# Performance work log

Hardware: AMD Instinct MI355X
Metric: run time of the kernel (lower is better)

Reference implementation:

```python
import jax, jax.numpy as jnp
import numpy as np

EPS = 1e-12

def t5_layer_norm(x, w):
    # T5-style RMS norm: no mean subtraction, no bias
    var = jnp.mean(x * x, axis=-1, keepdims=True)
    return x * jax.lax.rsqrt(var + EPS) * w

def gether(h, a2, t2):
    # a2: [B,S,1,1] (row similarity), t2: [B,1,S,1] (col similarity)
    h_y = h * t2
    h_left  = jnp.pad(h_y, ((0,0),(0,0),(1,0),(0,0)))[:, :, :-1, :]
    h_right = jnp.pad(h_y, ((0,0),(0,0),(0,1),(0,0)))[:, :, 1:, :]
    h_x = h * a2
    h_up   = jnp.pad(h_x, ((0,0),(1,0),(0,0),(0,0)))[:, :-1, :, :]
    h_down = jnp.pad(h_x, ((0,0),(0,1),(0,0),(0,0)))[:, 1:, :, :]
    return h + h_left + h_right + h_up + h_down

def syntax_gether(h, dep_weights):
    h_dep = h * dep_weights            # [B,S,S,D]
    h_in = jnp.sum(h_dep, axis=2)      # [B,S,D]
    h_out = jnp.sum(h_dep, axis=1)     # [B,S,D]
    return h_in[:, :, None, :] + h_out[:, None, :, :]

def feature_fusion(sem, syn, gate_w, gate_b):
    combined = jnp.concatenate([sem, syn], axis=-1)
    gate = jax.nn.sigmoid(combined @ gate_w + gate_b)
    return gate * sem + (1.0 - gate) * syn

def setup_inputs() -> dict:
    key = jax.random.key(0)
    ks = jax.random.split(key, 16)
    B, S, D_in, D_out = 4, 96, 768, 256
    N_DEP, D_DEP = 44, 6
    inp = {
        "table": jax.random.normal(ks[0], (B, S, S, D_in), dtype=jnp.float32),
        "a_simi": jax.random.uniform(ks[1], (B, S), dtype=jnp.float32),
        "t_simi": jax.random.uniform(ks[2], (B, S), dtype=jnp.float32),
        "dep_matrix": jax.random.randint(ks[3], (B, S, S), 0, 2).astype(jnp.float32),
        "dep_types": jax.random.randint(ks[4], (B, S, S), 0, N_DEP).astype(jnp.int32),
        # parameters (torch Linear weights stored transposed: [in, out])
        "dense1_w": jax.random.normal(ks[5], (D_in, D_in), dtype=jnp.float32) * 0.02,
        "dense1_b": jnp.zeros((D_in,), dtype=jnp.float32),
        "dense2_w": jax.random.normal(ks[6], (D_in, D_out), dtype=jnp.float32) * 0.02,
        "dense2_b": jnp.zeros((D_out,), dtype=jnp.float32),
        "dep_emb": jax.random.normal(ks[7], (N_DEP, D_DEP), dtype=jnp.float32) * 0.02,
        "dep_att_w": jax.random.normal(ks[8], (D_DEP, 1), dtype=jnp.float32) * 0.02,
        "dep_att_b": jnp.zeros((1,), dtype=jnp.float32),
        "gate_w": jax.random.normal(ks[9], (2 * D_in, D_in), dtype=jnp.float32) * 0.02,
        "gate_b": jnp.zeros((D_in,), dtype=jnp.float32),
        "norm1_w": jnp.ones((D_in,), dtype=jnp.float32),
        "norm2_w": jnp.ones((D_out,), dtype=jnp.float32),
    }
    return inp

def reference(table, a_simi, t_simi, dep_matrix, dep_types,
              dense1_w, dense1_b, dense2_w, dense2_b,
              dep_emb, dep_att_w, dep_att_b, gate_w, gate_b,
              norm1_w, norm2_w):
    a2 = a_simi[:, :, None, None]   # [B,S,1,1]
    t2 = t_simi[:, None, :, None]   # [B,1,S,1]
    dep_embeds = dep_emb[dep_types]                       # [B,S,S,6]
    dep_weights = jax.nn.sigmoid(dep_embeds @ dep_att_w + dep_att_b)
    dep_weights = dep_weights * dep_matrix[..., None]     # [B,S,S,1]

    h0 = table
    h1_sem = gether(h0, a2, t2)
    h1_syn = syntax_gether(h0, dep_weights)
    h1 = feature_fusion(h1_sem, h1_syn, gate_w, gate_b)
    h1 = jax.nn.relu(t5_layer_norm((h1 + h0) @ dense1_w + dense1_b, norm1_w))

    h2_sem = gether(h1, a2, t2)
    h2_syn = syntax_gether(h1, dep_weights)
    h2 = feature_fusion(h2_sem, h2_syn, gate_w, gate_b)
    h2 = jax.nn.relu(t5_layer_norm((h2 + h1) @ dense2_w + dense2_b, norm2_w))
    return h2
```

## Files before the change

kernel.cpp:

```cpp
#include <hip/hip_runtime.h>
#include <cstdint>
#include <cstddef>

#define SDIM 96
#define BDIM 4
#define NROWS (BDIM * SDIM * SDIM)
#define BSROWS (BDIM * SDIM)
#define DIN 768
#define DOUT 256

typedef short s16x8 __attribute__((ext_vector_type(8)));
typedef float f32x4 __attribute__((ext_vector_type(4)));
typedef unsigned short ushort_t;
typedef unsigned int uint_t;

__device__ __forceinline__ float sigmoid_f(float x) { return 1.0f / (1.0f + expf(-x)); }

__device__ __forceinline__ ushort_t f2bf(float x) {
    uint_t u = __float_as_uint(x);
    u = u + 0x7fffu + ((u >> 16) & 1u);
    return (ushort_t)(u >> 16);
}
__device__ __forceinline__ float bf2f(ushort_t h) {
    return __uint_as_float(((uint_t)h) << 16);
}

__device__ __forceinline__ void split_store(float x, ushort_t* __restrict__ ph,
                                            ushort_t* __restrict__ pl) {
    ushort_t h = f2bf(x);
    *ph = h;
    *pl = f2bf(x - bf2f(h));
}

__device__ __forceinline__ void load_lds16(const void* g, void* l) {
    __builtin_amdgcn_global_load_lds((const __attribute__((address_space(1))) uint_t*)g,
                                     (__attribute__((address_space(3))) uint_t*)l, 16, 0, 0);
}

__global__ __launch_bounds__(256) void depw_k(const int* __restrict__ types,
                                              const float* __restrict__ dmat,
                                              const float* __restrict__ emb,
                                              const float* __restrict__ aw,
                                              const float* __restrict__ ab,
                                              float* __restrict__ Wd) {
    int idx = blockIdx.x * 256 + threadIdx.x;
    if (idx >= NROWS) return;
    int t = types[idx];
    float s = ab[0];
#pragma unroll
    for (int k = 0; k < 6; ++k) s = fmaf(emb[t * 6 + k], aw[k], s);
    Wd[idx] = dmat[idx] * sigmoid_f(s);
}

__global__ __launch_bounds__(256) void splitT_k(const float* __restrict__ W,
                                                ushort_t* __restrict__ TH,
                                                ushort_t* __restrict__ TL, int K, int N) {
    int k = blockIdx.x * 256 + threadIdx.x;
    int n = blockIdx.y;
    if (k >= K) return;
    float x = W[(size_t)k * N + n];
    split_store(x, &TH[(size_t)n * K + k], &TL[(size_t)n * K + k]);
}

__global__ __launch_bounds__(256) void rowsum_k(const float* __restrict__ h,
                                                const float* __restrict__ W,
                                                float* __restrict__ hinF,
                                                ushort_t* __restrict__ hinH,
                                                ushort_t* __restrict__ hinL) {
    int d = blockIdx.x * 256 + threadIdx.x;
    int bi = blockIdx.y;
    const float* hp = h + (size_t)bi * SDIM * DIN + d;
    const float* wp = W + bi * SDIM;
    float acc = 0.f;
#pragma unroll 8
    for (int j = 0; j < SDIM; ++j) acc = fmaf(wp[j], hp[(size_t)j * DIN], acc);
    size_t o = (size_t)bi * DIN + d;
    hinF[o] = acc;
    split_store(acc, &hinH[o], &hinL[o]);
}

__global__ __launch_bounds__(256) void colsum_k(const float* __restrict__ h,
                                                const float* __restrict__ W,
                                                float* __restrict__ houtF,
                                                ushort_t* __restrict__ houtH,
                                                ushort_t* __restrict__ houtL) {
    int d = blockIdx.x * 256 + threadIdx.x;
    int bj = blockIdx.y;
    int b = bj / SDIM;
    int j = bj - b * SDIM;
    const float* hp = h + ((size_t)(b * SDIM) * SDIM + j) * DIN + d;
    const float* wp = W + (size_t)(b * SDIM) * SDIM + j;
    float acc = 0.f;
#pragma unroll 8
    for (int i = 0; i < SDIM; ++i)
        acc = fmaf(wp[(size_t)i * SDIM], hp[(size_t)i * SDIM * DIN], acc);
    size_t o = (size_t)bj * DIN + d;
    houtF[o] = acc;
    split_store(acc, &houtH[o], &houtL[o]);
}

__global__ __launch_bounds__(256) void sem_k(const float* __restrict__ h,
                                             const float* __restrict__ a_simi,
                                             const float* __restrict__ t_simi,
                                             ushort_t* __restrict__ semH,
                                             ushort_t* __restrict__ semL) {
    int idx = blockIdx.x * 256 + threadIdx.x;
    int d4 = idx % 192;
    int m = idx / 192;
    int j = m % SDIM;
    int r = m / SDIM;
    int i = r % SDIM;
    int b = r / SDIM;
    const float4* h4 = (const float4*)h;
    float4 acc = h4[(size_t)m * 192 + d4];
    if (j > 0) {
        float t = t_simi[b * SDIM + j - 1];
        float4 v = h4[(size_t)(m - 1) * 192 + d4];
        acc.x = fmaf(t, v.x, acc.x); acc.y = fmaf(t, v.y, acc.y);
        acc.z = fmaf(t, v.z, acc.z); acc.w = fmaf(t, v.w, acc.w);
    }
    if (j < SDIM - 1) {
        float t = t_simi[b * SDIM + j + 1];
        float4 v = h4[(size_t)(m + 1) * 192 + d4];
        acc.x = fmaf(t, v.x, acc.x); acc.y = fmaf(t, v.y, acc.y);
        acc.z = fmaf(t, v.z, acc.z); acc.w = fmaf(t, v.w, acc.w);
    }
    if (i > 0) {
        float a = a_simi[b * SDIM + i - 1];
        float4 v = h4[(size_t)(m - SDIM) * 192 + d4];
        acc.x = fmaf(a, v.x, acc.x); acc.y = fmaf(a, v.y, acc.y);
        acc.z = fmaf(a, v.z, acc.z); acc.w = fmaf(a, v.w, acc.w);
    }
    if (i < SDIM - 1) {
        float a = a_simi[b * SDIM + i + 1];
        float4 v = h4[(size_t)(m + SDIM) * 192 + d4];
        acc.x = fmaf(a, v.x, acc.x); acc.y = fmaf(a, v.y, acc.y);
        acc.z = fmaf(a, v.z, acc.z); acc.w = fmaf(a, v.w, acc.w);
    }
    size_t o = (size_t)m * DIN + d4 * 4;
    ushort_t hh[4], ll[4];
    float vv[4] = {acc.x, acc.y, acc.z, acc.w};
#pragma unroll
    for (int e = 0; e < 4; ++e) {
        hh[e] = f2bf(vv[e]);
        ll[e] = f2bf(vv[e] - bf2f(hh[e]));
    }
    *(ushort4*)&semH[o] = make_ushort4(hh[0], hh[1], hh[2], hh[3]);
    *(ushort4*)&semL[o] = make_ushort4(ll[0], ll[1], ll[2], ll[3]);
}

template <int EPI>
__global__ __launch_bounds__(256) void gemm_mfma(
    const ushort_t* __restrict__ AH, const ushort_t* __restrict__ AL,
    const ushort_t* __restrict__ BH, const ushort_t* __restrict__ BL,
    int M, int N, int K, int nbx,
    float* __restrict__ C, const float* __restrict__ bias,
    ushort_t* __restrict__ XH, ushort_t* __restrict__ XL,
    const float* __restrict__ Pin, const float* __restrict__ Pout,
    const float* __restrict__ hin, const float* __restrict__ hout,
    const float* __restrict__ hprev) {
    __shared__ __align__(16) ushort_t Ash[2][4096];
    __shared__ __align__(16) ushort_t Asl[2][4096];
    __shared__ __align__(16) ushort_t Bsh[2][4096];
    __shared__ __align__(16) ushort_t Bsl[2][4096];

    const int nwg = gridDim.x;
    const int orig = blockIdx.x;
    const int qq = nwg >> 3, rr = nwg & 7;
    const int xcd = orig & 7, sidx = orig >> 3;
    const int swz = (xcd < rr ? xcd * (qq + 1) : rr * (qq + 1) + (xcd - rr) * qq) + sidx;
    const int bx = swz % nbx;
    const int by = swz / nbx;
    const int bm = by * 128, bn = bx * 128;

    const int tid = threadIdx.x;
    const int wave = tid >> 6, lane = tid & 63;
    const int lq = lane & 15;
    const int lg = lane >> 4;
    const int wm = wave >> 1, wn = wave & 1;

    f32x4 acc[4][4];
#pragma unroll
    for (int a = 0; a < 4; ++a)
#pragma unroll
        for (int b = 0; b < 4; ++b) acc[a][b] = (f32x4){0.f, 0.f, 0.f, 0.f};

    const int nt = K >> 5;

#define STAGE(buf, k0)                                                              \
    {                                                                               \
        _Pragma("unroll") for (int cc = 0; cc < 2; ++cc) {                          \
            const int c = wave + cc * 4;                                            \
            const int row = c * 16 + lq;                                            \
            const size_t ga = (size_t)(bm + row) * K + (k0) + lg * 8;               \
            const size_t gb = (size_t)(bn + row) * K + (k0) + lg * 8;               \
            load_lds16(AH + ga, &Ash[buf][c * 512]);                                \
            load_lds16(AL + ga, &Asl[buf][c * 512]);                                \
            load_lds16(BH + gb, &Bsh[buf][c * 512]);                                \
            load_lds16(BL + gb, &Bsl[buf][c * 512]);                                \
        }                                                                           \
    }

    STAGE(0, 0);
    __syncthreads();

    int cur = 0;
    for (int t = 0; t < nt; ++t) {
        if (t + 1 < nt) STAGE(cur ^ 1, (t + 1) * 32);

        s16x8 ah[4], al[4], bh[4], bl[4];
#pragma unroll
        for (int f = 0; f < 4; ++f) {
            const int cA = (wm * 4 + f) * 512 + lane * 8;
            const int cB = (wn * 4 + f) * 512 + lane * 8;
            ah[f] = *(const s16x8*)&Ash[cur][cA];
            al[f] = *(const s16x8*)&Asl[cur][cA];
            bh[f] = *(const s16x8*)&Bsh[cur][cB];
            bl[f] = *(const s16x8*)&Bsl[cur][cB];
        }
        __builtin_amdgcn_s_setprio(1);
#pragma unroll
        for (int mf = 0; mf < 4; ++mf)
#pragma unroll
            for (int nf = 0; nf < 4; ++nf) {
                acc[mf][nf] = __builtin_amdgcn_mfma_f32_16x16x32_bf16(ah[mf], bh[nf], acc[mf][nf], 0, 0, 0);
                acc[mf][nf] = __builtin_amdgcn_mfma_f32_16x16x32_bf16(ah[mf], bl[nf], acc[mf][nf], 0, 0, 0);
                acc[mf][nf] = __builtin_amdgcn_mfma_f32_16x16x32_bf16(al[mf], bh[nf], acc[mf][nf], 0, 0, 0);
            }
        __builtin_amdgcn_s_setprio(0);
        __syncthreads();
        cur ^= 1;
    }
#undef STAGE

#pragma unroll
    for (int mf = 0; mf < 4; ++mf) {
#pragma unroll
        for (int jj = 0; jj < 4; ++jj) {
            const int gr = bm + wm * 64 + mf * 16 + lg * 4 + jj;
            int ri = 0, rj = 0;
            if (EPI == 1) {
                const int b_ = gr / 9216;
                const int rem = gr - b_ * 9216;
                const int i_ = rem / 96;
                const int j_ = rem - i_ * 96;
                ri = (b_ * 96 + i_) * 768;
                rj = (b_ * 96 + j_) * 768;
            }
#pragma unroll
            for (int nf = 0; nf < 4; ++nf) {
                const int gc = bn + wn * 64 + nf * 16 + lq;
                float v = acc[mf][nf][jj];
                if (EPI == 0) {
                    if (bias != nullptr) v += bias[gc];
                    C[(size_t)gr * N + gc] = v;
                } else {
                    const float gte = sigmoid_f(v + Pin[ri + gc] + Pout[rj + gc]);
                    const float syn = hin[ri + gc] + hout[rj + gc];
                    const size_t o = (size_t)gr * 768 + gc;
                    const float sem = bf2f(AH[o]) + bf2f(AL[o]);
                    const float x = fmaf(gte, sem - syn, syn) + hprev[o];
                    split_store(x, &XH[o], &XL[o]);
                }
            }
        }
    }
}

template <int D>
__global__ __launch_bounds__(256) void norm_relu_k(const float* __restrict__ Y,
                                                   const float* __restrict__ w,
                                                   float* __restrict__ out) {
    constexpr int E = D / 256;
    int row = blockIdx.x;
    int tid = threadIdx.x;
    float v[E];
    float ss = 0.f;
#pragma unroll
    for (int e = 0; e < E; ++e) {
        v[e] = Y[(size_t)row * D + e * 256 + tid];
        ss = fmaf(v[e], v[e], ss);
    }
#pragma unroll
    for (int off = 32; off >= 1; off >>= 1) ss += __shfl_down(ss, off);
    __shared__ float red[4];
    int lane = tid & 63;
    int wid = tid >> 6;
    if (lane == 0) red[wid] = ss;
    __syncthreads();
    float tot = red[0] + red[1] + red[2] + red[3];
    float scale = rsqrtf(tot / (float)D + 1e-12f);
#pragma unroll
    for (int e = 0; e < E; ++e) {
        float o = v[e] * scale * w[e * 256 + tid];
        out[(size_t)row * D + e * 256 + tid] = fmaxf(o, 0.f);
    }
}

extern "C" void kernel_launch(void* const* d_in, const int* in_sizes, int n_in,
                              void* d_out, int out_size, void* d_ws, size_t ws_size,
                              hipStream_t stream) {
    (void)in_sizes; (void)n_in; (void)out_size; (void)ws_size;
    const float* table = (const float*)d_in[0];
    const float* a_simi = (const float*)d_in[1];
    const float* t_simi = (const float*)d_in[2];
    const float* dep_matrix = (const float*)d_in[3];
    const int* dep_types = (const int*)d_in[4];
    const float* d1w = (const float*)d_in[5];
    const float* d1b = (const float*)d_in[6];
    const float* d2w = (const float*)d_in[7];
    const float* d2b = (const float*)d_in[8];
    const float* dep_emb = (const float*)d_in[9];
    const float* att_w = (const float*)d_in[10];
    const float* att_b = (const float*)d_in[11];
    const float* gate_w = (const float*)d_in[12];
    const float* gate_b = (const float*)d_in[13];
    const float* nw1 = (const float*)d_in[14];
    const float* nw2 = (const float*)d_in[15];
    float* out = (float*)d_out;

    char* ws = (char*)d_ws;
    size_t off = 0;
    float* Wd = (float*)(ws + off); off += 147456;
    float* hinF = (float*)(ws + off); off += 1179648;
    float* houtF = (float*)(ws + off); off += 1179648;
    float* Pin = (float*)(ws + off); off += 1179648;
    float* Pout = (float*)(ws + off); off += 1179648;
    ushort_t* hinH = (ushort_t*)(ws + off); off += 589824;
    ushort_t* hinL = (ushort_t*)(ws + off); off += 589824;
    ushort_t* houtH = (ushort_t*)(ws + off); off += 589824;
    ushort_t* houtL = (ushort_t*)(ws + off); off += 589824;
    ushort_t* GtopTH = (ushort_t*)(ws + off); off += 1179648;
    ushort_t* GtopTL = (ushort_t*)(ws + off); off += 1179648;
    ushort_t* GbotTH = (ushort_t*)(ws + off); off += 1179648;
    ushort_t* GbotTL = (ushort_t*)(ws + off); off += 1179648;
    ushort_t* D1TH = (ushort_t*)(ws + off); off += 1179648;
    ushort_t* D1TL = (ushort_t*)(ws + off); off += 1179648;
    ushort_t* D2TH = (ushort_t*)(ws + off); off += 393216;
    ushort_t* D2TL = (ushort_t*)(ws + off); off += 393216;
    char* P1 = ws + off; off += 113246208;
    char* P2 = ws + off; off += 113246208;
    char* P3 = ws + off; off += 113246208;

    const size_t HALF = 56623104;
    ushort_t* S1H = (ushort_t*)P1;            ushort_t* S1L = (ushort_t*)(P1 + HALF);
    ushort_t* X1H = (ushort_t*)P2;            ushort_t* X1L = (ushort_t*)(P2 + HALF);
    float* Y1 = (float*)P1;
    float* h1 = (float*)P3;
    ushort_t* S2H = (ushort_t*)P2;            ushort_t* S2L = (ushort_t*)(P2 + HALF);
    ushort_t* X2H = (ushort_t*)P1;            ushort_t* X2L = (ushort_t*)(P1 + HALF);
    float* Y2 = (float*)P3;

    const dim3 blk(256);
    const dim3 gSplit768(3, 768);
    const dim3 gSplit256(3, 256);
    const dim3 gRS(DIN / 256, BSROWS);
    const int gSem = (NROWS * (DIN / 4)) / 256;
    const int gBig = (NROWS / 128) * (DIN / 128);
    const int gD2g = (NROWS / 128) * (DOUT / 128);
    const int gP = (BSROWS / 128) * (DIN / 128);

    depw_k<<<NROWS / 256, blk, 0, stream>>>(dep_types, dep_matrix, dep_emb, att_w, att_b, Wd);
    splitT_k<<<gSplit768, blk, 0, stream>>>(gate_w, GtopTH, GtopTL, DIN, DIN);
    splitT_k<<<gSplit768, blk, 0, stream>>>(gate_w + (size_t)DIN * DIN, GbotTH, GbotTL, DIN, DIN);
    splitT_k<<<gSplit768, blk, 0, stream>>>(d1w, D1TH, D1TL, DIN, DIN);
    splitT_k<<<gSplit256, blk, 0, stream>>>(d2w, D2TH, D2TL, DIN, DOUT);

    rowsum_k<<<gRS, blk, 0, stream>>>(table, Wd, hinF, hinH, hinL);
    colsum_k<<<gRS, blk, 0, stream>>>(table, Wd, houtF, houtH, houtL);
    sem_k<<<gSem, blk, 0, stream>>>(table, a_simi, t_simi, S1H, S1L);
    gemm_mfma<0><<<gP, blk, 0, stream>>>(hinH, hinL, GbotTH, GbotTL, BSROWS, DIN, DIN, DIN / 128,
                                         Pin, gate_b, nullptr, nullptr, nullptr, nullptr, nullptr, nullptr, nullptr);
    gemm_mfma<0><<<gP, blk, 0, stream>>>(houtH, houtL, GbotTH, GbotTL, BSROWS, DIN, DIN, DIN / 128,
                                         Pout, nullptr, nullptr, nullptr, nullptr, nullptr, nullptr, nullptr, nullptr);
    gemm_mfma<1><<<gBig, blk, 0, stream>>>(S1H, S1L, GtopTH, GtopTL, NROWS, DIN, DIN, DIN / 128,
                                           nullptr, nullptr, X1H, X1L, Pin, Pout, hinF, houtF, table);
    gemm_mfma<0><<<gBig, blk, 0, stream>>>(X1H, X1L, D1TH, D1TL, NROWS, DIN, DIN, DIN / 128,
                                           Y1, d1b, nullptr, nullptr, nullptr, nullptr, nullptr, nullptr, nullptr);
    norm_relu_k<DIN><<<NROWS, blk, 0, stream>>>(Y1, nw1, h1);

    rowsum_k<<<gRS, blk, 0, stream>>>(h1, Wd, hinF, hinH, hinL);
    colsum_k<<<gRS, blk, 0, stream>>>(h1, Wd, houtF, houtH, houtL);
    sem_k<<<gSem, blk, 0, stream>>>(h1, a_simi, t_simi, S2H, S2L);
    gemm_mfma<0><<<gP, blk, 0, stream>>>(hinH, hinL, GbotTH, GbotTL, BSROWS, DIN, DIN, DIN / 128,
                                         Pin, gate_b, nullptr, nullptr, nullptr, nullptr, nullptr, nullptr, nullptr);
    gemm_mfma<0><<<gP, blk, 0, stream>>>(houtH, houtL, GbotTH, GbotTL, BSROWS, DIN, DIN, DIN / 128,
                                         Pout, nullptr, nullptr, nullptr, nullptr, nullptr, nullptr, nullptr, nullptr);
    gemm_mfma<1><<<gBig, blk, 0, stream>>>(S2H, S2L, GtopTH, GtopTL, NROWS, DIN, DIN, DIN / 128,
                                           nullptr, nullptr, X2H, X2L, Pin, Pout, hinF, houtF, h1);
    gemm_mfma<0><<<gD2g, blk, 0, stream>>>(X2H, X2L, D2TH, D2TL, NROWS, DOUT, DIN, DOUT / 128,
                                           Y2, d2b, nullptr, nullptr, nullptr, nullptr, nullptr, nullptr, nullptr);
    norm_relu_k<DOUT><<<NROWS, blk, 0, stream>>>(Y2, nw2, out);
}
```

Before: 1.525 ms.

## Use 256x128 GEMM tiles with 512 threads and merge Pin/Pout GEMMs

The MFMA GEMM tile grows from 128x128 to 256x128, with 512 threads (8 waves) per block, so each staged B tile is reused across twice as many A rows. The LDS double buffer is removed: the kernel now loads and syncs the same buffer every K-step. The separate Pin and Pout projection GEMMs are merged into one launch over stacked hin/hout rows, and the gate bias moves into the fused epilogue. This trades prefetch overlap for more operand reuse, and halves the block count of the large GEMMs, which may lower latency hiding and occupancy.

Result: slower. 1.642 ms (+7.7%).

```diff
diff --git a/kernel.cpp b/kernel.cpp
--- a/kernel.cpp
+++ b/kernel.cpp
@@ -150,7 +150,7 @@
 }
 
 template <int EPI>
-__global__ __launch_bounds__(256) void gemm_mfma(
+__global__ __launch_bounds__(512) void gemm_mfma(
     const ushort_t* __restrict__ AH, const ushort_t* __restrict__ AL,
     const ushort_t* __restrict__ BH, const ushort_t* __restrict__ BL,
     int M, int N, int K, int nbx,
@@ -159,10 +159,10 @@
     const float* __restrict__ Pin, const float* __restrict__ Pout,
     const float* __restrict__ hin, const float* __restrict__ hout,
     const float* __restrict__ hprev) {
-    __shared__ __align__(16) ushort_t Ash[2][4096];
-    __shared__ __align__(16) ushort_t Asl[2][4096];
-    __shared__ __align__(16) ushort_t Bsh[2][4096];
-    __shared__ __align__(16) ushort_t Bsl[2][4096];
+    __shared__ __align__(16) ushort_t Ash[8192];
+    __shared__ __align__(16) ushort_t Asl[8192];
+    __shared__ __align__(16) ushort_t Bsh[4096];
+    __shared__ __align__(16) ushort_t Bsl[4096];
 
     const int nwg = gridDim.x;
     const int orig = blockIdx.x;
@@ -171,7 +171,7 @@
     const int swz = (xcd < rr ? xcd * (qq + 1) : rr * (qq + 1) + (xcd - rr) * qq) + sidx;
     const int bx = swz % nbx;
     const int by = swz / nbx;
-    const int bm = by * 128, bn = bx * 128;
+    const int bm = by * 256, bn = bx * 128;
 
     const int tid = threadIdx.x;
     const int wave = tid >> 6, lane = tid & 63;
@@ -187,36 +187,36 @@
 
     const int nt = K >> 5;
 
-#define STAGE(buf, k0)                                                              \
+#define STAGE(k0)                                                                   \
     {                                                                               \
         _Pragma("unroll") for (int cc = 0; cc < 2; ++cc) {                          \
-            const int c = wave + cc * 4;                                            \
+            const int c = wave + cc * 8;                                            \
             const int row = c * 16 + lq;                                            \
             const size_t ga = (size_t)(bm + row) * K + (k0) + lg * 8;               \
-            const size_t gb = (size_t)(bn + row) * K + (k0) + lg * 8;               \
-            load_lds16(AH + ga, &Ash[buf][c * 512]);                                \
-            load_lds16(AL + ga, &Asl[buf][c * 512]);                                \
-            load_lds16(BH + gb, &Bsh[buf][c * 512]);                                \
-            load_lds16(BL + gb, &Bsl[buf][c * 512]);                                \
+            load_lds16(AH + ga, &Ash[c * 512]);                                     \
+            load_lds16(AL + ga, &Asl[c * 512]);                                     \
         }                                                                           \
-    }
-
-    STAGE(0, 0);
-    __syncthreads();
-
-    int cur = 0;
+        {                                                                           \
+            const int rowb = wave * 16 + lq;                                        \
+            const size_t gb = (size_t)(bn + rowb) * K + (k0) + lg * 8;              \
+            load_lds16(BH + gb, &Bsh[wave * 512]);                                  \
+            load_lds16(BL + gb, &Bsl[wave * 512]);                                  \
+        }                                                                           \
+    }
+
     for (int t = 0; t < nt; ++t) {
-        if (t + 1 < nt) STAGE(cur ^ 1, (t + 1) * 32);
+        STAGE(t * 32);
+        __syncthreads();
 
         s16x8 ah[4], al[4], bh[4], bl[4];
 #pragma unroll
         for (int f = 0; f < 4; ++f) {
             const int cA = (wm * 4 + f) * 512 + lane * 8;
             const int cB = (wn * 4 + f) * 512 + lane * 8;
-            ah[f] = *(const s16x8*)&Ash[cur][cA];
-            al[f] = *(const s16x8*)&Asl[cur][cA];
-            bh[f] = *(const s16x8*)&Bsh[cur][cB];
-            bl[f] = *(const s16x8*)&Bsl[cur][cB];
+            ah[f] = *(const s16x8*)&Ash[cA];
+            al[f] = *(const s16x8*)&Asl[cA];
+            bh[f] = *(const s16x8*)&Bsh[cB];
+            bl[f] = *(const s16x8*)&Bsl[cB];
         }
         __builtin_amdgcn_s_setprio(1);
 #pragma unroll
@@ -229,7 +229,6 @@
             }
         __builtin_amdgcn_s_setprio(0);
         __syncthreads();
-        cur ^= 1;
     }
 #undef STAGE
 
@@ -255,7 +254,7 @@
                     if (bias != nullptr) v += bias[gc];
                     C[(size_t)gr * N + gc] = v;
                 } else {
-                    const float gte = sigmoid_f(v + Pin[ri + gc] + Pout[rj + gc]);
+                    const float gte = sigmoid_f(v + Pin[ri + gc] + Pout[rj + gc] + bias[gc]);
                     const float syn = hin[ri + gc] + hout[rj + gc];
                     const size_t o = (size_t)gr * 768 + gc;
                     const float sem = bf2f(AH[o]) + bf2f(AL[o]);
@@ -324,12 +323,9 @@
     float* Wd = (float*)(ws + off); off += 147456;
     float* hinF = (float*)(ws + off); off += 1179648;
     float* houtF = (float*)(ws + off); off += 1179648;
-    float* Pin = (float*)(ws + off); off += 1179648;
-    float* Pout = (float*)(ws + off); off += 1179648;
-    ushort_t* hinH = (ushort_t*)(ws + off); off += 589824;
-    ushort_t* hinL = (ushort_t*)(ws + off); off += 589824;
-    ushort_t* houtH = (ushort_t*)(ws + off); off += 589824;
-    ushort_t* houtL = (ushort_t*)(ws + off); off += 589824;
+    float* Pfull = (float*)(ws + off); off += 2359296;
+    ushort_t* hioH = (ushort_t*)(ws + off); off += 1179648;
+    ushort_t* hioL = (ushort_t*)(ws + off); off += 1179648;
     ushort_t* GtopTH = (ushort_t*)(ws + off); off += 1179648;
     ushort_t* GtopTL = (ushort_t*)(ws + off); off += 1179648;
     ushort_t* GbotTH = (ushort_t*)(ws + off); off += 1179648;
@@ -351,14 +347,18 @@
     ushort_t* X2H = (ushort_t*)P1;            ushort_t* X2L = (ushort_t*)(P1 + HALF);
     float* Y2 = (float*)P3;
 
+    float* Pin = Pfull;
+    float* Pout = Pfull + (size_t)BSROWS * DIN;
+
     const dim3 blk(256);
+    const dim3 blk512(512);
     const dim3 gSplit768(3, 768);
     const dim3 gSplit256(3, 256);
     const dim3 gRS(DIN / 256, BSROWS);
     const int gSem = (NROWS * (DIN / 4)) / 256;
-    const int gBig = (NROWS / 128) * (DIN / 128);
-    const int gD2g = (NROWS / 128) * (DOUT / 128);
-    const int gP = (BSROWS / 128) * (DIN / 128);
+    const int gBig = (NROWS / 256) * (DIN / 128);
+    const int gD2g = (NROWS / 256) * (DOUT / 128);
+    const int gP = (2 * BSROWS / 256) * (DIN / 128);
 
     depw_k<<<NROWS / 256, blk, 0, stream>>>(dep_types, dep_matrix, dep_emb, att_w, att_b, Wd);
     splitT_k<<<gSplit768, blk, 0, stream>>>(gate_w, GtopTH, GtopTL, DIN, DIN);
@@ -366,29 +366,27 @@
     splitT_k<<<gSplit768, blk, 0, stream>>>(d1w, D1TH, D1TL, DIN, DIN);
     splitT_k<<<gSplit256, blk, 0, stream>>>(d2w, D2TH, D2TL, DIN, DOUT);
 
-    rowsum_k<<<gRS, blk, 0, stream>>>(table, Wd, hinF, hinH, hinL);
-    colsum_k<<<gRS, blk, 0, stream>>>(table, Wd, houtF, houtH, houtL);
+    rowsum_k<<<gRS, blk, 0, stream>>>(table, Wd, hinF, hioH, hioL);
+    colsum_k<<<gRS, blk, 0, stream>>>(table, Wd, houtF, hioH + (size_t)BSROWS * DIN,
+                                      hioL + (size_t)BSROWS * DIN);
     sem_k<<<gSem, blk, 0, stream>>>(table, a_simi, t_simi, S1H, S1L);
-    gemm_mfma<0><<<gP, blk, 0, stream>>>(hinH, hinL, GbotTH, GbotTL, BSROWS, DIN, DIN, DIN / 128,
-                                         Pin, gate_b, nullptr, nullptr, nullptr, nullptr, nullptr, nullptr, nullptr);
-    gemm_mfma<0><<<gP, blk, 0, stream>>>(houtH, houtL, GbotTH, GbotTL, BSROWS, DIN, DIN, DIN / 128,
-                                         Pout, nullptr, nullptr, nullptr, nullptr, nullptr, nullptr, nullptr, nullptr);
-    gemm_mfma<1><<<gBig, blk, 0, stream>>>(S1H, S1L, GtopTH, GtopTL, NROWS, DIN, DIN, DIN / 128,
-                                           nullptr, nullptr, X1H, X1L, Pin, Pout, hinF, houtF, table);
-    gemm_mfma<0><<<gBig, blk, 0, stream>>>(X1H, X1L, D1TH, D1TL, NROWS, DIN, DIN, DIN / 128,
-                                           Y1, d1b, nullptr, nullptr, nullptr, nullptr, nullptr, nullptr, nullptr);
+    gemm_mfma<0><<<gP, blk512, 0, stream>>>(hioH, hioL, GbotTH, GbotTL, 2 * BSROWS, DIN, DIN, DIN / 128,
+                                            Pfull, nullptr, nullptr, nullptr, nullptr, nullptr, nullptr, nullptr, nullptr);
+    gemm_mfma<1><<<gBig, blk512, 0, stream>>>(S1H, S1L, GtopTH, GtopTL, NROWS, DIN, DIN, DIN / 128,
+                                              nullptr, gate_b, X1H, X1L, Pin, Pout, hinF, houtF, table);
+    gemm_mfma<0><<<gBig, blk512, 0, stream>>>(X1H, X1L, D1TH, D1TL, NROWS, DIN, DIN, DIN / 128,
+                                              Y1, d1b, nullptr, nullptr, nullptr, nullptr, nullptr, nullptr, nullptr);
     norm_relu_k<DIN><<<NROWS, blk, 0, stream>>>(Y1, nw1, h1);
 
-    rowsum_k<<<gRS, blk, 0, stream>>>(h1, Wd, hinF, hinH, hinL);
-    colsum_k<<<gRS, blk, 0, stream>>>(h1, Wd, houtF, houtH, houtL);
+    rowsum_k<<<gRS, blk, 0, stream>>>(h1, Wd, hinF, hioH, hioL);
+    colsum_k<<<gRS, blk, 0, stream>>>(h1, Wd, houtF, hioH + (size_t)BSROWS * DIN,
+                                      hioL + (size_t)BSROWS * DIN);
     sem_k<<<gSem, blk, 0, stream>>>(h1, a_simi, t_simi, S2H, S2L);
-    gemm_mfma<0><<<gP, blk, 0, stream>>>(hinH, hinL, GbotTH, GbotTL, BSROWS, DIN, DIN, DIN / 128,
-                                         Pin, gate_b, nullptr, nullptr, nullptr, nullptr, nullptr, nullptr, nullptr);
-    gemm_mfma<0><<<gP, blk, 0, stream>>>(houtH, houtL, GbotTH, GbotTL, BSROWS, DIN, DIN, DIN / 128,
-                                         Pout, nullptr, nullptr, nullptr, nullptr, nullptr, nullptr, nullptr, nullptr);
-    gemm_mfma<1><<<gBig, blk, 0, stream>>>(S2H, S2L, GtopTH, GtopTL, NROWS, DIN, DIN, DIN / 128,
-                                           nullptr, nullptr, X2H, X2L, Pin, Pout, hinF, houtF, h1);
-    gemm_mfma<0><<<gD2g, blk, 0, stream>>>(X2H, X2L, D2TH, D2TL, NROWS, DOUT, DIN, DOUT / 128,
-                                           Y2, d2b, nullptr, nullptr, nullptr, nullptr, nullptr, nullptr, nullptr);
+    gemm_mfma<0><<<gP, blk512, 0, stream>>>(hioH, hioL, GbotTH, GbotTL, 2 * BSROWS, DIN, DIN, DIN / 128,
+                                            Pfull, nullptr, nullptr, nullptr, nullptr, nullptr, nullptr, nullptr, nullptr);
+    gemm_mfma<1><<<gBig, blk512, 0, stream>>>(S2H, S2L, GtopTH, GtopTL, NROWS, DIN, DIN, DIN / 128,
+                                              nullptr, gate_b, X2H, X2L, Pin, Pout, hinF, houtF, h1);
+    gemm_mfma<0><<<gD2g, blk512, 0, stream>>>(X2H, X2L, D2TH, D2TL, NROWS, DOUT, DIN, DOUT / 128,
+                                              Y2, d2b, nullptr, nullptr, nullptr, nullptr, nullptr, nullptr, nullptr);
     norm_relu_k<DOUT><<<NROWS, blk, 0, stream>>>(Y2, nw2, out);
 }
```
